# Performance work log

Measured on AMD Instinct MI355X. Metric: run time of the kernel, lower is better.

Reference implementation:

```python
import jax, jax.numpy as jnp
import numpy as np

B, N, D = 32, 128, 64
E = N * N
EPS = 1e-5


def _bn(x, gamma, beta):
    # torch BatchNorm1d on (B, C, D): normalize per-channel over (batch, last dim)
    mean = jnp.mean(x, axis=(0, 2), keepdims=True)
    var = jnp.var(x, axis=(0, 2), keepdims=True)
    return (x - mean) * jax.lax.rsqrt(var + EPS) * gamma[None, :, None] + beta[None, :, None]


def _gat_layer(x, edge, Wh, We, Wp, Wa, gv, bv, ge, be):
    b, n, d = x.shape
    res = x
    z_h = jnp.einsum('bnd,od->bno', x, Wh)   # fc_h (torch Linear: y = x W^T)
    z_e = jnp.einsum('bed,od->beo', edge, We)  # fc_e
    # incidence matmuls are pure gathers: edge e = i*n + j
    z_src = jnp.broadcast_to(z_h[:, None, :, :], (b, n, n, d)).reshape(b, n * n, d)  # start: edge (i,j) <- node j
    z_dst = jnp.broadcast_to(z_h[:, :, None, :], (b, n, n, d)).reshape(b, n * n, d)  # end:   edge (i,j) <- node i
    z = jnp.concatenate([z_src, z_dst, z_e], axis=-1)  # (b, E, 3d)
    z_e_new = jnp.einsum('bec,oc->beo', z, Wp)  # fc_proj
    attn = jnp.einsum('bec,c->be', z, Wa[0])    # attn_fc -> (b, E)
    attn = jnp.where(attn >= 0, attn, 0.01 * attn)  # LeakyReLU(0.01)
    attn = jax.nn.softmax(attn.reshape(b, n, n), axis=2).reshape(b, n * n)  # softmax over sources j
    # scatter via end^T: node i <- sum_j attn[i,j] * z_src[i*n+j]
    agg = (attn[:, :, None] * z_src).reshape(b, n, n, d).sum(axis=2)
    x_new = jax.nn.elu(res + _bn(agg, gv, bv))
    edge_new = jax.nn.elu(_bn(z_e_new, ge, be))
    return x_new, edge_new


def setup_inputs():
    key = jax.random.key(0)
    ks = jax.random.split(key, 10)
    scale = float(np.sqrt(2.0 / D))
    return {
        'x': jax.random.normal(ks[0], (B, N, D), jnp.float32),
        'edge': jax.random.normal(ks[1], (B, E, D), jnp.float32),
        'Wh1': jax.random.normal(ks[2], (D, D), jnp.float32) * scale,
        'We1': jax.random.normal(ks[3], (D, D), jnp.float32) * scale,
        'Wp1': jax.random.normal(ks[4], (D, 3 * D), jnp.float32) * scale,
        'Wa1': jax.random.normal(ks[5], (1, 3 * D), jnp.float32) * scale,
        'Wh2': jax.random.normal(ks[6], (D, D), jnp.float32) * scale,
        'We2': jax.random.normal(ks[7], (D, D), jnp.float32) * scale,
        'Wp2': jax.random.normal(ks[8], (D, 3 * D), jnp.float32) * scale,
        'Wa2': jax.random.normal(ks[9], (1, 3 * D), jnp.float32) * scale,
        'gv1': jnp.ones((N,), jnp.float32), 'bv1': jnp.zeros((N,), jnp.float32),
        'ge1': jnp.ones((E,), jnp.float32), 'be1': jnp.zeros((E,), jnp.float32),
        'gv2': jnp.ones((N,), jnp.float32), 'bv2': jnp.zeros((N,), jnp.float32),
        'ge2': jnp.ones((E,), jnp.float32), 'be2': jnp.zeros((E,), jnp.float32),
    }


def reference(x, edge, Wh1, We1, Wp1, Wa1, Wh2, We2, Wp2, Wa2,
              gv1, bv1, ge1, be1, gv2, bv2, ge2, be2):
    x, edge = _gat_layer(x, edge, Wh1, We1, Wp1, Wa1, gv1, bv1, ge1, be1)
    x, edge = _gat_layer(x, edge, Wh2, We2, Wp2, Wa2, gv2, bv2, ge2, be2)
    return x, edge
```

## Files before the change

kernel.cpp:

```cpp
#include <hip/hip_runtime.h>
#include <math.h>

#define BB 32
#define NN 128
#define DD 64
#define EE (NN*NN)
#define EPSI 1e-5f

typedef __attribute__((ext_vector_type(8))) short bf16x8;
typedef __attribute__((ext_vector_type(4))) short s16x4;
typedef __attribute__((ext_vector_type(4))) float f32x4;

#define LGKM0() do { asm volatile("s_waitcnt lgkmcnt(0)" ::: "memory"); \
                     __builtin_amdgcn_sched_barrier(0); } while (0)

#define DPPADD(v, ctrl, rmask)                                               \
    (v) += __int_as_float(__builtin_amdgcn_update_dpp(                       \
               0, __float_as_int(v), (ctrl), (rmask), 0xf, true))

__device__ __forceinline__ float wave_sum64(float v) {
    DPPADD(v, 0x111, 0xf);
    DPPADD(v, 0x112, 0xf);
    DPPADD(v, 0x114, 0xf);
    DPPADD(v, 0x118, 0xf);
    DPPADD(v, 0x142, 0xa);
    DPPADD(v, 0x143, 0xc);
    return __int_as_float(__builtin_amdgcn_readlane(__float_as_int(v), 63));
}

__device__ __forceinline__ short f2bf(float f) {
    union { float f; unsigned u; } v; v.f = f;
    unsigned u = v.u;
    unsigned r = (u + 0x7FFFu + ((u >> 16) & 1u)) >> 16;
    return (short)r;
}
__device__ __forceinline__ float elu(float v) {
    return v > 0.f ? v : __expf(v) - 1.f;
}

__global__ void k_node(const float* __restrict__ x, const float* __restrict__ Wh,
                       const float* __restrict__ Wp, const float* __restrict__ We,
                       const float* __restrict__ Wa,
                       float* __restrict__ zh, float* __restrict__ PsT,
                       float* __restrict__ PdT, float* __restrict__ sO,
                       float* __restrict__ tO,
                       short* __restrict__ MbT, short* __restrict__ wfT)
{
    const int row = blockIdx.x;
    const int d = threadIdx.x;
    if (row >= BB*NN) {
        const int ff = row - BB*NN;
        float acc = 0.f;
        for (int o = 0; o < DD; ++o)
            acc += Wp[ff*192 + 128 + o] * We[o*DD + d];
        MbT[(((ff >> 4)*2 + (d >> 5))*64 + (ff & 15) + ((d >> 3) & 3)*16)*8 + (d & 7)]
            = f2bf(acc);
        if (ff == 0) {
            for (int q = 0; q < 16; ++q) wfT[d*16 + q] = 0;
            __syncthreads();
            float aw = 0.f;
            for (int o = 0; o < DD; ++o)
                aw += Wa[128 + o] * We[o*DD + d];
            wfT[((d >> 5)*64 + ((d >> 3) & 3)*16)*8 + (d & 7)] = f2bf(aw);
        }
        return;
    }
    const int b = row >> 7, n = row & 127;
    __shared__ float xr[DD];
    __shared__ float zr[DD];
    xr[d] = x[row*DD + d];
    __syncthreads();
    float acc = 0.f;
#pragma unroll
    for (int k = 0; k < DD; ++k) acc += xr[k] * Wh[d*DD + k];
    zr[d] = acc;
    zh[row*DD + d] = acc;
    __syncthreads();
    float a0 = 0.f, a1 = 0.f;
#pragma unroll
    for (int o = 0; o < DD; ++o) {
        float z = zr[o];
        a0 += Wp[d*192 + o]      * z;
        a1 += Wp[d*192 + 64 + o] * z;
    }
    const int fi = ((b >> 4)*4 + (d >> 4))*256 + (((b >> 2) & 3)*16 + (d & 15))*4 + (b & 3);
    PsT[n*2048 + fi] = a0;
    PdT[n*2048 + fi] = a1;
    float sv = zr[d] * Wa[d];
    float tv = zr[d] * Wa[64 + d];
#pragma unroll
    for (int off = 32; off; off >>= 1) {
        sv += __shfl_xor(sv, off);
        tv += __shfl_xor(tv, off);
    }
    if (d == 0) { sO[row] = sv; tO[row] = tv; }
}

template <int INM, int OUTM>
__global__ __launch_bounds__(256, 4) void k_edge(
    const void* einv,
    const short* __restrict__ MbT,
    const short* __restrict__ wfT,
    const float* __restrict__ PsT,
    const float* __restrict__ PdT,
    const float* __restrict__ ge, const float* __restrict__ be,
    void* eoutv, float* __restrict__ uout)
{
    __shared__ __align__(16) char SM[4][8704];
    const int t  = threadIdx.x;
    const int l  = t & 63;
    const int wv = t >> 6;
    const int lr = l & 15;
    const int lg = l >> 4;
    const int e  = blockIdx.x * 4 + wv;
    const int i0 = e >> 7, j0 = e & 127;
    short (*As)[72] = reinterpret_cast<short (*)[72]>(&SM[wv][0]);
    float (*Z)[68]  = reinterpret_cast<float (*)[68]>(&SM[wv][0]);

    bf16x8 afr[2][2];
    if constexpr (INM == 0) {
        const float* ein = (const float*)einv;
        float4 sv[8];
#pragma unroll
        for (int it = 0; it < 8; ++it) {
            const int b = 4*it + (l >> 4);
            sv[it] = *reinterpret_cast<const float4*>(
                         ein + ((size_t)b*EE + e)*DD + (l & 15)*4);
        }
#pragma unroll
        for (int it = 0; it < 8; ++it) {
            const int b = 4*it + (l >> 4);
            s16x4 o;
            o[0] = f2bf(sv[it].x); o[1] = f2bf(sv[it].y);
            o[2] = f2bf(sv[it].z); o[3] = f2bf(sv[it].w);
            *reinterpret_cast<s16x4*>(&As[b][(l & 15)*4]) = o;
        }
        LGKM0();
#pragma unroll
        for (int m = 0; m < 2; ++m)
#pragma unroll
            for (int s = 0; s < 2; ++s)
                afr[m][s] = *reinterpret_cast<const bf16x8*>(
                                &As[16*m + lr][s*32 + lg*8]);
    } else {
        const short* ein = (const short*)einv + (size_t)e*BB*DD;
#pragma unroll
        for (int m = 0; m < 2; ++m)
#pragma unroll
            for (int s = 0; s < 2; ++s)
                afr[m][s] = *reinterpret_cast<const bf16x8*>(
                                ein + ((m*2 + s)*64 + l)*8);
    }

    bf16x8 bfr[4][2];
#pragma unroll
    for (int n = 0; n < 4; ++n)
#pragma unroll
        for (int s = 0; s < 2; ++s)
            bfr[n][s] = *reinterpret_cast<const bf16x8*>(MbT + ((n*2 + s)*64 + l)*8);
    bf16x8 wfrag[2];
#pragma unroll
    for (int s = 0; s < 2; ++s)
        wfrag[s] = *reinterpret_cast<const bf16x8*>(wfT + (s*64 + l)*8);

    f32x4 acc[2][4];
    f32x4 uacc[2];
    {
        const float* psb = PsT + j0*2048;
        const float* pdb = PdT + i0*2048;
#pragma unroll
        for (int m = 0; m < 2; ++m) {
            uacc[m] = (f32x4){0.f, 0.f, 0.f, 0.f};
#pragma unroll
            for (int n = 0; n < 4; ++n) {
                const float4 a = *reinterpret_cast<const float4*>(psb + (m*4+n)*256 + l*4);
                const float4 c = *reinterpret_cast<const float4*>(pdb + (m*4+n)*256 + l*4);
                acc[m][n] = (f32x4){a.x+c.x, a.y+c.y, a.z+c.z, a.w+c.w};
            }
        }
    }

#pragma unroll
    for (int m = 0; m < 2; ++m) {
#pragma unroll
        for (int n = 0; n < 4; ++n)
            acc[m][n] = __builtin_amdgcn_mfma_f32_16x16x32_bf16(afr[m][0], bfr[n][0], acc[m][n], 0, 0, 0);
        uacc[m] = __builtin_amdgcn_mfma_f32_16x16x32_bf16(afr[m][0], wfrag[0], uacc[m], 0, 0, 0);
#pragma unroll
        for (int n = 0; n < 4; ++n)
            acc[m][n] = __builtin_amdgcn_mfma_f32_16x16x32_bf16(afr[m][1], bfr[n][1], acc[m][n], 0, 0, 0);
        uacc[m] = __builtin_amdgcn_mfma_f32_16x16x32_bf16(afr[m][1], wfrag[1], uacc[m], 0, 0, 0);
    }

    float s1 = 0.f, s2 = 0.f;
#pragma unroll
    for (int m = 0; m < 2; ++m)
#pragma unroll
        for (int n = 0; n < 4; ++n)
#pragma unroll
            for (int q = 0; q < 4; ++q) { float v = acc[m][n][q]; s1 += v; s2 += v*v; }
    s1 = wave_sum64(s1);
    s2 = wave_sum64(s2);
    const float mean = s1 * (1.f/2048.f);
    const float var  = s2 * (1.f/2048.f) - mean*mean;
    const float sc = ge[e] * rsqrtf(var + EPSI);
    const float sh = be[e] - mean*sc;

#pragma unroll
    for (int m = 0; m < 2; ++m)
#pragma unroll
        for (int n = 0; n < 4; ++n)
#pragma unroll
            for (int q = 0; q < 4; ++q)
                acc[m][n][q] = elu(acc[m][n][q]*sc + sh);

    if (lr == 0) {
#pragma unroll
        for (int m = 0; m < 2; ++m)
#pragma unroll
            for (int q = 0; q < 4; ++q)
                uout[(size_t)(16*m + 4*lg + q)*EE + e] = uacc[m][q];
    }

    LGKM0();
#pragma unroll
    for (int m = 0; m < 2; ++m)
#pragma unroll
        for (int n = 0; n < 4; ++n)
#pragma unroll
            for (int q = 0; q < 4; ++q)
                Z[16*m + 4*lg + q][16*n + lr] = acc[m][n][q];
    LGKM0();
    if constexpr (OUTM == 0) {
        float* eout = (float*)eoutv;
#pragma unroll
        for (int it = 0; it < 8; ++it) {
            const int b = lg + 4*it;
            float4 z = *reinterpret_cast<float4*>(&Z[b][lr*4]);
            *reinterpret_cast<float4*>(eout + ((size_t)b*EE + e)*DD + lr*4) = z;
        }
    } else {
        short* eoutp = (short*)eoutv + (size_t)e*BB*DD;
#pragma unroll
        for (int it = 0; it < 4; ++it) {
            const int b  = (l >> 3) + 8*it;
            const int c0 = (l & 7)*8;
            float4 zlo = *reinterpret_cast<float4*>(&Z[b][c0]);
            float4 zhi = *reinterpret_cast<float4*>(&Z[b][c0+4]);
            bf16x8 o;
            o[0]=f2bf(zlo.x); o[1]=f2bf(zlo.y); o[2]=f2bf(zlo.z); o[3]=f2bf(zlo.w);
            o[4]=f2bf(zhi.x); o[5]=f2bf(zhi.y); o[6]=f2bf(zhi.z); o[7]=f2bf(zhi.w);
            const int sp = (l & 7) >> 2;
            const int lp = (b & 15) + ((l & 3) << 4);
            *reinterpret_cast<bf16x8*>(eoutp + (((b >> 4)*2 + sp)*64 + lp)*8) = o;
        }
    }
}

__global__ void k_attn(const float* __restrict__ sI, const float* __restrict__ tI,
                       const float* __restrict__ u, const float* __restrict__ zh,
                       float* __restrict__ agg)
{
    int blk = blockIdx.x; int b = blk >> 7, i = blk & 127;
    int l = threadIdx.x;
    __shared__ float at[NN];
    float ti = tI[blk];
    float l0 = sI[b*NN + l]      + ti + u[b*EE + i*NN + l];
    float l1 = sI[b*NN + l + 64] + ti + u[b*EE + i*NN + l + 64];
    l0 = l0 >= 0.f ? l0 : 0.01f*l0;
    l1 = l1 >= 0.f ? l1 : 0.01f*l1;
    float mx = fmaxf(l0, l1);
#pragma unroll
    for (int off = 32; off; off >>= 1) mx = fmaxf(mx, __shfl_xor(mx, off));
    float e0 = __expf(l0 - mx), e1 = __expf(l1 - mx);
    float sm = e0 + e1;
#pragma unroll
    for (int off = 32; off; off >>= 1) sm += __shfl_xor(sm, off);
    float inv = 1.f / sm;
    at[l]      = e0 * inv;
    at[l + 64] = e1 * inv;
    __syncthreads();
    const float* zb = zh + (size_t)b*NN*DD + l;
    float a0 = 0.f, a1 = 0.f, a2 = 0.f, a3 = 0.f;
#pragma unroll 4
    for (int j = 0; j < NN; j += 4) {
        a0 += at[j]     * zb[(j)    *DD];
        a1 += at[j + 1] * zb[(j + 1)*DD];
        a2 += at[j + 2] * zb[(j + 2)*DD];
        a3 += at[j + 3] * zb[(j + 3)*DD];
    }
    agg[(b*NN + i)*DD + l] = (a0 + a1) + (a2 + a3);
}

__global__ void k_vbn(const float* __restrict__ agg, const float* __restrict__ xres,
                      const float* __restrict__ gv, const float* __restrict__ bv,
                      float* __restrict__ xout)
{
    int i = blockIdx.x, t = threadIdx.x;
    float vals[8];
    float s1 = 0.f, s2 = 0.f;
#pragma unroll
    for (int q = 0; q < 8; ++q) {
        int m = t + 256*q; int b = m >> 6, d = m & 63;
        float v = agg[(b*NN + i)*DD + d];
        vals[q] = v; s1 += v; s2 += v*v;
    }
#pragma unroll
    for (int off = 1; off < 64; off <<= 1) {
        s1 += __shfl_xor(s1, off);
        s2 += __shfl_xor(s2, off);
    }
    __shared__ float r1[4], r2[4];
    int wv = t >> 6;
    if ((t & 63) == 0) { r1[wv] = s1; r2[wv] = s2; }
    __syncthreads();
    s1 = r1[0] + r1[1] + r1[2] + r1[3];
    s2 = r2[0] + r2[1] + r2[2] + r2[3];
    float mean  = s1 * (1.f/2048.f);
    float var   = s2 * (1.f/2048.f) - mean*mean;
    float scale = gv[i] * rsqrtf(var + EPSI);
    float shift = bv[i] - mean*scale;
#pragma unroll
    for (int q = 0; q < 8; ++q) {
        int m = t + 256*q; int b = m >> 6, d = m & 63;
        float v = vals[q]*scale + shift + xres[(b*NN + i)*DD + d];
        xout[(b*NN + i)*DD + d] = v > 0.f ? v : __expf(v) - 1.f;
    }
}

extern "C" void kernel_launch(void* const* d_in, const int* in_sizes, int n_in,
                              void* d_out, int out_size, void* d_ws, size_t ws_size,
                              hipStream_t stream)
{
    const float* x    = (const float*)d_in[0];
    const float* edge = (const float*)d_in[1];
    const float* Wh1  = (const float*)d_in[2];
    const float* We1  = (const float*)d_in[3];
    const float* Wp1  = (const float*)d_in[4];
    const float* Wa1  = (const float*)d_in[5];
    const float* Wh2  = (const float*)d_in[6];
    const float* We2  = (const float*)d_in[7];
    const float* Wp2  = (const float*)d_in[8];
    const float* Wa2  = (const float*)d_in[9];
    const float* gv1  = (const float*)d_in[10];
    const float* bv1  = (const float*)d_in[11];
    const float* ge1  = (const float*)d_in[12];
    const float* be1  = (const float*)d_in[13];
    const float* gv2  = (const float*)d_in[14];
    const float* bv2  = (const float*)d_in[15];
    const float* ge2  = (const float*)d_in[16];
    const float* be2  = (const float*)d_in[17];

    float* xout = (float*)d_out;
    float* eout = (float*)d_out + BB*NN*DD;

    float* ws  = (float*)d_ws;
    short* MbT = (short*)ws;  ws += DD*DD/2;
    short* wfT = (short*)ws;  ws += 1024/2;
    float* zh  = ws;  ws += BB*NN*DD;
    float* PsT = ws;  ws += NN*BB*DD;
    float* PdT = ws;  ws += NN*BB*DD;
    float* sb  = ws;  ws += BB*NN;
    float* tb  = ws;  ws += BB*NN;
    float* ub  = ws;  ws += BB*EE;
    float* agg = ws;  ws += BB*NN*DD;
    float* x1  = ws;  ws += BB*NN*DD;
    short* ebf = (short*)ws;
    const size_t need = ((size_t)(ws - (float*)d_ws))*4 + (size_t)EE*BB*DD*2;

    const bool dense = (ws_size >= need);

    k_node<<<BB*NN + 64, 64, 0, stream>>>(x, Wh1, Wp1, We1, Wa1, zh, PsT, PdT, sb, tb, MbT, wfT);
    if (dense)
        k_edge<0,1><<<EE/4, 256, 0, stream>>>(edge, MbT, wfT, PsT, PdT, ge1, be1, ebf, ub);
    else
        k_edge<0,0><<<EE/4, 256, 0, stream>>>(edge, MbT, wfT, PsT, PdT, ge1, be1, eout, ub);
    k_attn<<<BB*NN, 64, 0, stream>>>(sb, tb, ub, zh, agg);
    k_vbn<<<NN, 256, 0, stream>>>(agg, x, gv1, bv1, x1);
    k_node<<<BB*NN + 64, 64, 0, stream>>>(x1, Wh2, Wp2, We2, Wa2, zh, PsT, PdT, sb, tb, MbT, wfT);
    if (dense)
        k_edge<1,0><<<EE/4, 256, 0, stream>>>(ebf, MbT, wfT, PsT, PdT, ge2, be2, eout, ub);
    else
        k_edge<0,0><<<EE/4, 256, 0, stream>>>(eout, MbT, wfT, PsT, PdT, ge2, be2, eout, ub);
    k_attn<<<BB*NN, 64, 0, stream>>>(sb, tb, ub, zh, agg);
    k_vbn<<<NN, 256, 0, stream>>>(agg, x1, gv2, bv2, xout);
}
```

Measured before the change: 187.6 us.

## Restructure edge kernel per batch-row with split BN stats and deferred normalize

The edge kernel now assigns each block to one batch and one destination row, so edge features are read and written contiguously rather than strided across the batch. Edge BatchNorm statistics become per-(edge,batch) partial sums, reduced by a small finalize kernel into scale and shift. The layer-1 BN+ELU is applied on the fly when layer 2 loads its bf16 intermediate, and layer-2 output goes through a separate finalize pass into fp32. The aim is to replace batch-strided memory access with streaming access. The cost is extra kernel launches, an extra bf16 round trip for the layer-2 output, and new partial-sum buffers.

Result: slower. 210.2 us (+12.1%).

```diff
diff --git a/kernel.cpp b/kernel.cpp
--- a/kernel.cpp
+++ b/kernel.cpp
@@ -14,26 +14,16 @@
 #define LGKM0() do { asm volatile("s_waitcnt lgkmcnt(0)" ::: "memory"); \
                      __builtin_amdgcn_sched_barrier(0); } while (0)
 
-#define DPPADD(v, ctrl, rmask)                                               \
-    (v) += __int_as_float(__builtin_amdgcn_update_dpp(                       \
-               0, __float_as_int(v), (ctrl), (rmask), 0xf, true))
-
-__device__ __forceinline__ float wave_sum64(float v) {
-    DPPADD(v, 0x111, 0xf);
-    DPPADD(v, 0x112, 0xf);
-    DPPADD(v, 0x114, 0xf);
-    DPPADD(v, 0x118, 0xf);
-    DPPADD(v, 0x142, 0xa);
-    DPPADD(v, 0x143, 0xc);
-    return __int_as_float(__builtin_amdgcn_readlane(__float_as_int(v), 63));
-}
-
 __device__ __forceinline__ short f2bf(float f) {
     union { float f; unsigned u; } v; v.f = f;
     unsigned u = v.u;
     unsigned r = (u + 0x7FFFu + ((u >> 16) & 1u)) >> 16;
     return (short)r;
 }
+__device__ __forceinline__ float bf2f(short s) {
+    union { unsigned u; float f; } v; v.u = ((unsigned)(unsigned short)s) << 16;
+    return v.f;
+}
 __device__ __forceinline__ float elu(float v) {
     return v > 0.f ? v : __expf(v) - 1.f;
 }
@@ -41,9 +31,10 @@
 __global__ void k_node(const float* __restrict__ x, const float* __restrict__ Wh,
                        const float* __restrict__ Wp, const float* __restrict__ We,
                        const float* __restrict__ Wa,
-                       float* __restrict__ zh, float* __restrict__ PsT,
-                       float* __restrict__ PdT, float* __restrict__ sO,
-                       float* __restrict__ tO,
+                       float* __restrict__ zh,
+                       float* __restrict__ PsJ, float* __restrict__ PdP,
+                       float* __restrict__ PsT, float* __restrict__ PdT,
+                       float* __restrict__ sO, float* __restrict__ tO,
                        short* __restrict__ MbT, short* __restrict__ wfT)
 {
     const int row = blockIdx.x;
@@ -83,6 +74,11 @@
         a0 += Wp[d*192 + o]      * z;
         a1 += Wp[d*192 + 64 + o] * z;
     }
+    {
+        const int rt = n & 15;
+        PsJ[(((b*8 + (n >> 4))*4 + (d >> 4))*64 + (rt >> 2)*16 + (d & 15))*4 + (rt & 3)] = a0;
+        PdP[row*DD + d] = a1;
+    }
     const int fi = ((b >> 4)*4 + (d >> 4))*256 + (((b >> 2) & 3)*16 + (d & 15))*4 + (b & 3);
     PsT[n*2048 + fi] = a0;
     PdT[n*2048 + fi] = a1;
@@ -96,15 +92,17 @@
     if (d == 0) { sO[row] = sv; tO[row] = tv; }
 }
 
-template <int INM, int OUTM>
-__global__ __launch_bounds__(256, 4) void k_edge(
+template <int LP>
+__global__ __launch_bounds__(256, 4) void k_eb(
     const void* einv,
     const short* __restrict__ MbT,
     const short* __restrict__ wfT,
-    const float* __restrict__ PsT,
-    const float* __restrict__ PdT,
-    const float* __restrict__ ge, const float* __restrict__ be,
-    void* eoutv, float* __restrict__ uout)
+    const float* __restrict__ PsJ,
+    const float* __restrict__ PdP,
+    const float* __restrict__ sc1, const float* __restrict__ sh1,
+    float* __restrict__ sps, float* __restrict__ spq,
+    short* __restrict__ zout,
+    float* __restrict__ uout)
 {
     __shared__ __align__(16) char SM[4][8704];
     const int t  = threadIdx.x;
@@ -112,46 +110,213 @@
     const int wv = t >> 6;
     const int lr = l & 15;
     const int lg = l >> 4;
-    const int e  = blockIdx.x * 4 + wv;
+    const int b  = blockIdx.x >> 7;
+    const int i0 = blockIdx.x & 127;
+    const int e0w = i0*128 + wv*32;
+    short (*As)[72] = reinterpret_cast<short (*)[72]>(&SM[wv][0]);
+    float (*Z)[68]  = reinterpret_cast<float (*)[68]>(&SM[wv][0]);
+
+    if constexpr (LP == 0) {
+        const float* base = (const float*)einv + ((size_t)b*EE + e0w)*DD;
+        float4 sv[8];
+#pragma unroll
+        for (int it = 0; it < 8; ++it)
+            sv[it] = *reinterpret_cast<const float4*>(base + it*256 + l*4);
+#pragma unroll
+        for (int it = 0; it < 8; ++it) {
+            const int r  = it*4 + (l >> 4);
+            const int d0 = (l & 15)*4;
+            s16x4 o;
+            o[0] = f2bf(sv[it].x); o[1] = f2bf(sv[it].y);
+            o[2] = f2bf(sv[it].z); o[3] = f2bf(sv[it].w);
+            *reinterpret_cast<s16x4*>(&As[r][d0]) = o;
+        }
+    } else {
+        const short* base = (const short*)einv + ((size_t)b*EE + e0w)*DD;
+#pragma unroll
+        for (int it = 0; it < 4; ++it) {
+            const int r  = (l >> 3) + 8*it;
+            const int d0 = (l & 7)*8;
+            bf16x8 v = *reinterpret_cast<const bf16x8*>(base + r*DD + d0);
+            const float scv = sc1[e0w + r], shv = sh1[e0w + r];
+            bf16x8 o;
+#pragma unroll
+            for (int j = 0; j < 8; ++j)
+                o[j] = f2bf(elu(bf2f(v[j])*scv + shv));
+            *reinterpret_cast<bf16x8*>(&As[r][d0]) = o;
+        }
+    }
+    LGKM0();
+
+    bf16x8 afr[2][2];
+#pragma unroll
+    for (int m = 0; m < 2; ++m)
+#pragma unroll
+        for (int s = 0; s < 2; ++s)
+            afr[m][s] = *reinterpret_cast<const bf16x8*>(&As[16*m + lr][s*32 + lg*8]);
+
+    bf16x8 bfr[4][2];
+#pragma unroll
+    for (int n = 0; n < 4; ++n)
+#pragma unroll
+        for (int s = 0; s < 2; ++s)
+            bfr[n][s] = *reinterpret_cast<const bf16x8*>(MbT + ((n*2 + s)*64 + l)*8);
+    bf16x8 wfrag[2];
+#pragma unroll
+    for (int s = 0; s < 2; ++s)
+        wfrag[s] = *reinterpret_cast<const bf16x8*>(wfT + (s*64 + l)*8);
+
+    f32x4 acc[2][4];
+    f32x4 uacc[2];
+    float pd[4];
+#pragma unroll
+    for (int n = 0; n < 4; ++n)
+        pd[n] = PdP[((size_t)(b*NN + i0))*DD + 16*n + lr];
+#pragma unroll
+    for (int m = 0; m < 2; ++m) {
+        uacc[m] = (f32x4){0.f, 0.f, 0.f, 0.f};
+        const int jb = wv*2 + m;
+#pragma unroll
+        for (int n = 0; n < 4; ++n) {
+            const float4 p = *reinterpret_cast<const float4*>(
+                PsJ + (((b*8 + jb)*4 + n)*64 + l)*4);
+            acc[m][n] = (f32x4){p.x + pd[n], p.y + pd[n], p.z + pd[n], p.w + pd[n]};
+        }
+    }
+
+#pragma unroll
+    for (int m = 0; m < 2; ++m) {
+#pragma unroll
+        for (int n = 0; n < 4; ++n)
+            acc[m][n] = __builtin_amdgcn_mfma_f32_16x16x32_bf16(afr[m][0], bfr[n][0], acc[m][n], 0, 0, 0);
+        uacc[m] = __builtin_amdgcn_mfma_f32_16x16x32_bf16(afr[m][0], wfrag[0], uacc[m], 0, 0, 0);
+#pragma unroll
+        for (int n = 0; n < 4; ++n)
+            acc[m][n] = __builtin_amdgcn_mfma_f32_16x16x32_bf16(afr[m][1], bfr[n][1], acc[m][n], 0, 0, 0);
+        uacc[m] = __builtin_amdgcn_mfma_f32_16x16x32_bf16(afr[m][1], wfrag[1], uacc[m], 0, 0, 0);
+    }
+
+    if (lr == 0) {
+#pragma unroll
+        for (int m = 0; m < 2; ++m)
+#pragma unroll
+            for (int q = 0; q < 4; ++q)
+                uout[(size_t)b*EE + e0w + 16*m + 4*lg + q] = uacc[m][q];
+    }
+
+#pragma unroll
+    for (int m = 0; m < 2; ++m)
+#pragma unroll
+        for (int q = 0; q < 4; ++q) {
+            float v  = acc[m][0][q] + acc[m][1][q] + acc[m][2][q] + acc[m][3][q];
+            float vv = acc[m][0][q]*acc[m][0][q] + acc[m][1][q]*acc[m][1][q]
+                     + acc[m][2][q]*acc[m][2][q] + acc[m][3][q]*acc[m][3][q];
+#pragma unroll
+            for (int off = 1; off < 16; off <<= 1) {
+                v  += __shfl_xor(v, off);
+                vv += __shfl_xor(vv, off);
+            }
+            if (lr == 0) {
+                const int e = e0w + 16*m + 4*lg + q;
+                sps[(size_t)e*BB + b] = v;
+                spq[(size_t)e*BB + b] = vv;
+            }
+        }
+
+    LGKM0();
+#pragma unroll
+    for (int m = 0; m < 2; ++m)
+#pragma unroll
+        for (int n = 0; n < 4; ++n)
+#pragma unroll
+            for (int q = 0; q < 4; ++q)
+                Z[16*m + 4*lg + q][16*n + lr] = acc[m][n][q];
+    LGKM0();
+    short* zo = zout + ((size_t)b*EE + e0w)*DD;
+#pragma unroll
+    for (int it = 0; it < 4; ++it) {
+        const int r  = (l >> 3) + 8*it;
+        const int c0 = (l & 7)*8;
+        float4 zlo = *reinterpret_cast<float4*>(&Z[r][c0]);
+        float4 zhi = *reinterpret_cast<float4*>(&Z[r][c0+4]);
+        bf16x8 o;
+        o[0]=f2bf(zlo.x); o[1]=f2bf(zlo.y); o[2]=f2bf(zlo.z); o[3]=f2bf(zlo.w);
+        o[4]=f2bf(zhi.x); o[5]=f2bf(zhi.y); o[6]=f2bf(zhi.z); o[7]=f2bf(zhi.w);
+        *reinterpret_cast<bf16x8*>(zo + r*DD + c0) = o;
+    }
+}
+
+__global__ void k_fs(const float* __restrict__ sps, const float* __restrict__ spq,
+                     const float* __restrict__ g, const float* __restrict__ be,
+                     float* __restrict__ sc, float* __restrict__ sh)
+{
+    const int e = blockIdx.x * 256 + threadIdx.x;
+    float s = 0.f, q = 0.f;
+#pragma unroll
+    for (int k = 0; k < BB; k += 4) {
+        const float4 a = *reinterpret_cast<const float4*>(sps + (size_t)e*BB + k);
+        const float4 c = *reinterpret_cast<const float4*>(spq + (size_t)e*BB + k);
+        s += (a.x + a.y) + (a.z + a.w);
+        q += (c.x + c.y) + (c.z + c.w);
+    }
+    const float mean = s * (1.f/2048.f);
+    const float var  = q * (1.f/2048.f) - mean*mean;
+    const float scv  = g[e] * rsqrtf(var + EPSI);
+    sc[e] = scv;
+    sh[e] = be[e] - mean*scv;
+}
+
+__global__ __launch_bounds__(256) void k_fin(const short* __restrict__ z,
+                                             const float* __restrict__ sc,
+                                             const float* __restrict__ sh,
+                                             float* __restrict__ eout)
+{
+    const size_t base = ((size_t)blockIdx.x * 256 + threadIdx.x) * 8;
+    const int e = (int)((base >> 6) & (EE - 1));
+    const bf16x8 v = *reinterpret_cast<const bf16x8*>(z + base);
+    const float scv = sc[e], shv = sh[e];
+    float4 o0, o1;
+    o0.x = elu(bf2f(v[0])*scv + shv); o0.y = elu(bf2f(v[1])*scv + shv);
+    o0.z = elu(bf2f(v[2])*scv + shv); o0.w = elu(bf2f(v[3])*scv + shv);
+    o1.x = elu(bf2f(v[4])*scv + shv); o1.y = elu(bf2f(v[5])*scv + shv);
+    o1.z = elu(bf2f(v[6])*scv + shv); o1.w = elu(bf2f(v[7])*scv + shv);
+    *reinterpret_cast<float4*>(eout + base)     = o0;
+    *reinterpret_cast<float4*>(eout + base + 4) = o1;
+}
+
+__global__ __launch_bounds__(256, 4) void k_edge_f(
+    const float* ein, const short* __restrict__ MbT, const short* __restrict__ wfT,
+    const float* __restrict__ PsT, const float* __restrict__ PdT,
+    const float* __restrict__ ge, const float* __restrict__ be,
+    float* eout, float* __restrict__ uout)
+{
+    __shared__ __align__(16) char SM[4][8704];
+    const int t = threadIdx.x, l = t & 63, wv = t >> 6;
+    const int lr = l & 15, lg = l >> 4;
+    const int e = blockIdx.x * 4 + wv;
     const int i0 = e >> 7, j0 = e & 127;
     short (*As)[72] = reinterpret_cast<short (*)[72]>(&SM[wv][0]);
     float (*Z)[68]  = reinterpret_cast<float (*)[68]>(&SM[wv][0]);
-
+    float4 sv[8];
+#pragma unroll
+    for (int it = 0; it < 8; ++it) {
+        const int b = 4*it + (l >> 4);
+        sv[it] = *reinterpret_cast<const float4*>(ein + ((size_t)b*EE + e)*DD + (l & 15)*4);
+    }
+#pragma unroll
+    for (int it = 0; it < 8; ++it) {
+        const int b = 4*it + (l >> 4);
+        s16x4 o;
+        o[0]=f2bf(sv[it].x); o[1]=f2bf(sv[it].y); o[2]=f2bf(sv[it].z); o[3]=f2bf(sv[it].w);
+        *reinterpret_cast<s16x4*>(&As[b][(l & 15)*4]) = o;
+    }
+    LGKM0();
     bf16x8 afr[2][2];
-    if constexpr (INM == 0) {
-        const float* ein = (const float*)einv;
-        float4 sv[8];
-#pragma unroll
-        for (int it = 0; it < 8; ++it) {
-            const int b = 4*it + (l >> 4);
-            sv[it] = *reinterpret_cast<const float4*>(
-                         ein + ((size_t)b*EE + e)*DD + (l & 15)*4);
-        }
-#pragma unroll
-        for (int it = 0; it < 8; ++it) {
-            const int b = 4*it + (l >> 4);
-            s16x4 o;
-            o[0] = f2bf(sv[it].x); o[1] = f2bf(sv[it].y);
-            o[2] = f2bf(sv[it].z); o[3] = f2bf(sv[it].w);
-            *reinterpret_cast<s16x4*>(&As[b][(l & 15)*4]) = o;
-        }
-        LGKM0();
-#pragma unroll
-        for (int m = 0; m < 2; ++m)
-#pragma unroll
-            for (int s = 0; s < 2; ++s)
-                afr[m][s] = *reinterpret_cast<const bf16x8*>(
-                                &As[16*m + lr][s*32 + lg*8]);
-    } else {
-        const short* ein = (const short*)einv + (size_t)e*BB*DD;
-#pragma unroll
-        for (int m = 0; m < 2; ++m)
-#pragma unroll
-            for (int s = 0; s < 2; ++s)
-                afr[m][s] = *reinterpret_cast<const bf16x8*>(
-                                ein + ((m*2 + s)*64 + l)*8);
-    }
-
+#pragma unroll
+    for (int m = 0; m < 2; ++m)
+#pragma unroll
+        for (int s = 0; s < 2; ++s)
+            afr[m][s] = *reinterpret_cast<const bf16x8*>(&As[16*m + lr][s*32 + lg*8]);
     bf16x8 bfr[4][2];
 #pragma unroll
     for (int n = 0; n < 4; ++n)
@@ -162,15 +327,13 @@
 #pragma unroll
     for (int s = 0; s < 2; ++s)
         wfrag[s] = *reinterpret_cast<const bf16x8*>(wfT + (s*64 + l)*8);
-
-    f32x4 acc[2][4];
-    f32x4 uacc[2];
+    f32x4 acc[2][4]; f32x4 uacc[2];
     {
         const float* psb = PsT + j0*2048;
         const float* pdb = PdT + i0*2048;
 #pragma unroll
         for (int m = 0; m < 2; ++m) {
-            uacc[m] = (f32x4){0.f, 0.f, 0.f, 0.f};
+            uacc[m] = (f32x4){0.f,0.f,0.f,0.f};
 #pragma unroll
             for (int n = 0; n < 4; ++n) {
                 const float4 a = *reinterpret_cast<const float4*>(psb + (m*4+n)*256 + l*4);
@@ -179,7 +342,6 @@
             }
         }
     }
-
 #pragma unroll
     for (int m = 0; m < 2; ++m) {
 #pragma unroll
@@ -191,7 +353,6 @@
             acc[m][n] = __builtin_amdgcn_mfma_f32_16x16x32_bf16(afr[m][1], bfr[n][1], acc[m][n], 0, 0, 0);
         uacc[m] = __builtin_amdgcn_mfma_f32_16x16x32_bf16(afr[m][1], wfrag[1], uacc[m], 0, 0, 0);
     }
-
     float s1 = 0.f, s2 = 0.f;
 #pragma unroll
     for (int m = 0; m < 2; ++m)
@@ -199,13 +360,15 @@
         for (int n = 0; n < 4; ++n)
 #pragma unroll
             for (int q = 0; q < 4; ++q) { float v = acc[m][n][q]; s1 += v; s2 += v*v; }
-    s1 = wave_sum64(s1);
-    s2 = wave_sum64(s2);
+#pragma unroll
+    for (int off = 1; off < 64; off <<= 1) {
+        s1 += __shfl_xor(s1, off);
+        s2 += __shfl_xor(s2, off);
+    }
     const float mean = s1 * (1.f/2048.f);
     const float var  = s2 * (1.f/2048.f) - mean*mean;
     const float sc = ge[e] * rsqrtf(var + EPSI);
     const float sh = be[e] - mean*sc;
-
 #pragma unroll
     for (int m = 0; m < 2; ++m)
 #pragma unroll
@@ -213,7 +376,6 @@
 #pragma unroll
             for (int q = 0; q < 4; ++q)
                 acc[m][n][q] = elu(acc[m][n][q]*sc + sh);
-
     if (lr == 0) {
 #pragma unroll
         for (int m = 0; m < 2; ++m)
@@ -221,7 +383,6 @@
             for (int q = 0; q < 4; ++q)
                 uout[(size_t)(16*m + 4*lg + q)*EE + e] = uacc[m][q];
     }
-
     LGKM0();
 #pragma unroll
     for (int m = 0; m < 2; ++m)
@@ -231,29 +392,11 @@
             for (int q = 0; q < 4; ++q)
                 Z[16*m + 4*lg + q][16*n + lr] = acc[m][n][q];
     LGKM0();
-    if constexpr (OUTM == 0) {
-        float* eout = (float*)eoutv;
-#pragma unroll
-        for (int it = 0; it < 8; ++it) {
-            const int b = lg + 4*it;
-            float4 z = *reinterpret_cast<float4*>(&Z[b][lr*4]);
-            *reinterpret_cast<float4*>(eout + ((size_t)b*EE + e)*DD + lr*4) = z;
-        }
-    } else {
-        short* eoutp = (short*)eoutv + (size_t)e*BB*DD;
-#pragma unroll
-        for (int it = 0; it < 4; ++it) {
-            const int b  = (l >> 3) + 8*it;
-            const int c0 = (l & 7)*8;
-            float4 zlo = *reinterpret_cast<float4*>(&Z[b][c0]);
-            float4 zhi = *reinterpret_cast<float4*>(&Z[b][c0+4]);
-            bf16x8 o;
-            o[0]=f2bf(zlo.x); o[1]=f2bf(zlo.y); o[2]=f2bf(zlo.z); o[3]=f2bf(zlo.w);
-            o[4]=f2bf(zhi.x); o[5]=f2bf(zhi.y); o[6]=f2bf(zhi.z); o[7]=f2bf(zhi.w);
-            const int sp = (l & 7) >> 2;
-            const int lp = (b & 15) + ((l & 3) << 4);
-            *reinterpret_cast<bf16x8*>(eoutp + (((b >> 4)*2 + sp)*64 + lp)*8) = o;
-        }
+#pragma unroll
+    for (int it = 0; it < 8; ++it) {
+        const int b = lg + 4*it;
+        float4 z = *reinterpret_cast<float4*>(&Z[b][lr*4]);
+        *reinterpret_cast<float4*>(eout + ((size_t)b*EE + e)*DD + lr*4) = z;
     }
 }
 
@@ -358,6 +501,8 @@
     short* MbT = (short*)ws;  ws += DD*DD/2;
     short* wfT = (short*)ws;  ws += 1024/2;
     float* zh  = ws;  ws += BB*NN*DD;
+    float* PsJ = ws;  ws += BB*NN*DD;
+    float* PdP = ws;  ws += BB*NN*DD;
     float* PsT = ws;  ws += NN*BB*DD;
     float* PdT = ws;  ws += NN*BB*DD;
     float* sb  = ws;  ws += BB*NN;
@@ -365,23 +510,32 @@
     float* ub  = ws;  ws += BB*EE;
     float* agg = ws;  ws += BB*NN*DD;
     float* x1  = ws;  ws += BB*NN*DD;
-    short* ebf = (short*)ws;
-    const size_t need = ((size_t)(ws - (float*)d_ws))*4 + (size_t)EE*BB*DD*2;
+    float* sps = ws;  ws += EE*BB;
+    float* spq = ws;  ws += EE*BB;
+    float* sc  = ws;  ws += EE;
+    float* sh  = ws;  ws += EE;
+    short* z12 = (short*)ws;
+    const size_t need = ((size_t)(ws - (float*)d_ws))*4 + (size_t)BB*EE*DD*2;
 
     const bool dense = (ws_size >= need);
 
-    k_node<<<BB*NN + 64, 64, 0, stream>>>(x, Wh1, Wp1, We1, Wa1, zh, PsT, PdT, sb, tb, MbT, wfT);
-    if (dense)
-        k_edge<0,1><<<EE/4, 256, 0, stream>>>(edge, MbT, wfT, PsT, PdT, ge1, be1, ebf, ub);
-    else
-        k_edge<0,0><<<EE/4, 256, 0, stream>>>(edge, MbT, wfT, PsT, PdT, ge1, be1, eout, ub);
+    k_node<<<BB*NN + 64, 64, 0, stream>>>(x, Wh1, Wp1, We1, Wa1, zh, PsJ, PdP, PsT, PdT, sb, tb, MbT, wfT);
+    if (dense) {
+        k_eb<0><<<BB*128, 256, 0, stream>>>(edge, MbT, wfT, PsJ, PdP, nullptr, nullptr, sps, spq, z12, ub);
+        k_fs<<<EE/256, 256, 0, stream>>>(sps, spq, ge1, be1, sc, sh);
+    } else {
+        k_edge_f<<<EE/4, 256, 0, stream>>>(edge, MbT, wfT, PsT, PdT, ge1, be1, eout, ub);
+    }
     k_attn<<<BB*NN, 64, 0, stream>>>(sb, tb, ub, zh, agg);
     k_vbn<<<NN, 256, 0, stream>>>(agg, x, gv1, bv1, x1);
-    k_node<<<BB*NN + 64, 64, 0, stream>>>(x1, Wh2, Wp2, We2, Wa2, zh, PsT, PdT, sb, tb, MbT, wfT);
-    if (dense)
-        k_edge<1,0><<<EE/4, 256, 0, stream>>>(ebf, MbT, wfT, PsT, PdT, ge2, be2, eout, ub);
-    else
-        k_edge<0,0><<<EE/4, 256, 0, stream>>>(eout, MbT, wfT, PsT, PdT, ge2, be2, eout, ub);
+    k_node<<<BB*NN + 64, 64, 0, stream>>>(x1, Wh2, Wp2, We2, Wa2, zh, PsJ, PdP, PsT, PdT, sb, tb, MbT, wfT);
+    if (dense) {
+        k_eb<1><<<BB*128, 256, 0, stream>>>(z12, MbT, wfT, PsJ, PdP, sc, sh, sps, spq, z12, ub);
+        k_fs<<<EE/256, 256, 0, stream>>>(sps, spq, ge2, be2, sc, sh);
+        k_fin<<<16384, 256, 0, stream>>>(z12, sc, sh, eout);
+    } else {
+        k_edge_f<<<EE/4, 256, 0, stream>>>(eout, MbT, wfT, PsT, PdT, ge2, be2, eout, ub);
+    }
     k_attn<<<BB*NN, 64, 0, stream>>>(sb, tb, ub, zh, agg);
     k_vbn<<<NN, 256, 0, stream>>>(agg, x1, gv2, bv2, xout);
 }
```
